# Performance work log

Hardware: AMD Instinct MI355X
Metric: run time of the kernel (lower is better)

The kernel has to match this reference:

```python
import jax, jax.numpy as jnp
from jax import lax
import numpy as np

RATIOS = (0.5, 1.0, 2.0)
SCALES = (8, 16, 32)
BASE = 16
STRIDE = 16
IMG_H, IMG_W = 1024, 1024
NMS_THR = 0.7
N_IN = 6000   # eval mode (training=False)
N_OUT = 300
MIN_SIZE = 16


def _base_anchors():
    ctr = BASE / 2.0
    anc = []
    for r in RATIOS:
        for s in SCALES:
            h = BASE * s * np.sqrt(r)
            w = BASE * s * np.sqrt(1.0 / r)
            anc.append([ctr - h / 2, ctr - w / 2, ctr + h / 2, ctr + w / 2])
    return np.asarray(anc, dtype=np.float32)  # (9,4) yxyx


def _shifted_anchors(H, W):
    base = _base_anchors()
    sy = np.arange(H, dtype=np.float32) * STRIDE
    sx = np.arange(W, dtype=np.float32) * STRIDE
    yy, xx = np.meshgrid(sy, sx, indexing='ij')
    shift = np.stack([yy, xx, yy, xx], axis=-1).reshape(-1, 1, 4)  # (H*W,1,4)
    return jnp.asarray((shift + base[None]).reshape(-1, 4))        # (H*W*9,4)


def _conv(x, w, b):
    y = lax.conv_general_dilated(x, w, (1, 1), 'SAME',
                                 dimension_numbers=('NCHW', 'OIHW', 'NCHW'))
    return y + b[None, :, None, None]


def _loc2bbox(src, locs):
    h = src[:, 2] - src[:, 0]
    w = src[:, 3] - src[:, 1]
    cy = src[:, 0] + 0.5 * h
    cx = src[:, 1] + 0.5 * w
    dy, dx, dh, dw = locs[:, 0], locs[:, 1], locs[:, 2], locs[:, 3]
    cty = dy * h + cy
    ctx = dx * w + cx
    th = jnp.exp(dh) * h
    tw = jnp.exp(dw) * w
    return jnp.stack([cty - 0.5 * th, ctx - 0.5 * tw,
                      cty + 0.5 * th, ctx + 0.5 * tw], axis=-1)


def _nms_keep(boxes, valid):
    n = boxes.shape[0]
    areas = (boxes[:, 2] - boxes[:, 0]) * (boxes[:, 3] - boxes[:, 1])
    idx = jnp.arange(n)

    def body(i, keep):
        b = lax.dynamic_slice(boxes, (i, 0), (1, 4))[0]
        yy1 = jnp.maximum(b[0], boxes[:, 0])
        xx1 = jnp.maximum(b[1], boxes[:, 1])
        yy2 = jnp.minimum(b[2], boxes[:, 2])
        xx2 = jnp.minimum(b[3], boxes[:, 3])
        inter = jnp.clip(yy2 - yy1, 0) * jnp.clip(xx2 - xx1, 0)
        iou = inter / (areas[i] + areas - inter + 1e-9)
        sup = (iou > NMS_THR) & (idx > i) & keep[i]
        return keep & ~sup

    return lax.fori_loop(0, n, body, valid)


def _proposals(locs, fg, anchors):
    # locs (R,4), fg (R,), anchors (R,4) -> (N_OUT,4) padded with zeros
    rois = _loc2bbox(anchors, locs)
    y1 = jnp.clip(rois[:, 0], 0, IMG_H)
    y2 = jnp.clip(rois[:, 2], 0, IMG_H)
    x1 = jnp.clip(rois[:, 1], 0, IMG_W)
    x2 = jnp.clip(rois[:, 3], 0, IMG_W)
    rois = jnp.stack([y1, x1, y2, x2], axis=-1)
    valid = ((y2 - y1) >= MIN_SIZE) & ((x2 - x1) >= MIN_SIZE)
    s = jnp.where(valid, fg, -jnp.inf)
    order = jnp.argsort(-s)[:N_IN]
    rois_s = rois[order]
    valid_s = valid[order]
    keep = _nms_keep(rois_s, valid_s)
    rank = jnp.cumsum(keep.astype(jnp.int32)) - 1
    tgt = jnp.where(keep & (rank < N_OUT), rank, N_OUT)
    out = jnp.zeros((N_OUT + 1, 4), rois.dtype).at[tgt].set(rois_s)
    return out[:N_OUT]


def reference(x, conv_w, conv_b, score_w, score_b, loc_w, loc_b):
    B, C, H, W = x.shape
    anchors = _shifted_anchors(H, W)                      # (R,4)
    h = jax.nn.relu(_conv(x, conv_w, conv_b))             # (B,mid,H,W)
    rpn_locs = _conv(h, loc_w, loc_b).transpose(0, 2, 3, 1).reshape(B, -1, 4)
    rpn_scores = _conv(h, score_w, score_b).transpose(0, 2, 3, 1).reshape(B, -1, 2)
    fg = jax.nn.softmax(rpn_scores, axis=2)[:, :, 1]      # (B,R)
    rois = jax.vmap(_proposals, in_axes=(0, 0, None))(rpn_locs, fg, anchors)
    rois = rois.reshape(-1, 4)                            # (B*N_OUT,4)
    roi_indices = jnp.repeat(jnp.arange(B, dtype=jnp.int32), N_OUT)
    return rpn_scores, rpn_locs, rois, roi_indices, anchors


def setup_inputs() -> dict:
    key = jax.random.key(0)
    ks = jax.random.split(key, 7)
    B, Cin, Cmid, H, W = 4, 512, 512, 64, 64
    return {
        'x': jax.random.normal(ks[0], (B, Cin, H, W), jnp.float32),
        'conv_w': jax.random.normal(ks[1], (Cmid, Cin, 3, 3), jnp.float32) * 0.01,
        'conv_b': jax.random.normal(ks[2], (Cmid,), jnp.float32) * 0.01,
        'score_w': jax.random.normal(ks[3], (18, Cmid, 1, 1), jnp.float32) * 0.01,
        'score_b': jax.random.normal(ks[4], (18,), jnp.float32) * 0.01,
        'loc_w': jax.random.normal(ks[5], (36, Cmid, 1, 1), jnp.float32) * 0.01,
        'loc_b': jax.random.normal(ks[6], (36,), jnp.float32) * 0.01,
    }
```

## Files before the change

### kernel.cpp

```cpp
#include <hip/hip_runtime.h>
#include <cstdint>
#include <cmath>

namespace {
constexpr int BATCH = 4;
constexpr int CIN   = 512;
constexpr int CMID  = 512;
constexpr int HSZ   = 64, WSZ = 64, HWP = 4096;
constexpr int NA    = 36864;
constexpr int NIN_  = 6000;
constexpr int NOUT2 = 300;
constexpr int NW    = 94;

constexpr size_t O_SC  = 0;
constexpr size_t O_LC  = 294912;
constexpr size_t O_ROI = 884736;
constexpr size_t O_IDX = 889536;
constexpr size_t O_ANC = 890736;

constexpr size_t W_H    = 0;
constexpr size_t W_WHI  = 8388608;
constexpr size_t W_WLO  = 9568256;
constexpr size_t W_R4   = 0;
constexpr size_t W_SK   = 589824;
constexpr size_t W_HIST = 737280;
constexpr size_t W_CNT  = 753664;
constexpr size_t W_CUT  = 753668;
constexpr size_t W_NHI1 = 753672;
constexpr size_t W_CUT2 = 753676;
constexpr size_t W_NHI2 = 753680;
constexpr size_t W_CUT3 = 753684;
constexpr size_t W_ZERO = 753688;
constexpr size_t W_NHI3 = 753692;
constexpr size_t W_H2   = 753728;
constexpr size_t W_H3   = 770112;
constexpr size_t W_CKEY = 901184;
constexpr size_t W_RS   = 1196096;
constexpr size_t W_VS   = 1292096;
constexpr size_t W_MAT  = 1316096;
}

typedef _Float16 f16;
typedef __attribute__((ext_vector_type(4))) _Float16 f16x4;
typedef __attribute__((ext_vector_type(8))) _Float16 f16x8;
typedef __attribute__((ext_vector_type(4))) float f32x4;

__global__ __launch_bounds__(256) void k0w(const float* __restrict__ w,
                                           f16* __restrict__ whi, f16* __restrict__ wlo) {
    int o = blockIdx.x * 256 + threadIdx.x;
    int ci = o & 511;
    int r  = o >> 9;
    int co = r & 511;
    int kk = r >> 9;
    float f = w[(co * CIN + ci) * 9 + kk] * 64.0f;
    f16 hv = (f16)f;
    whi[o] = hv;
    wlo[o] = (f16)((f - (float)hv) * 2048.0f);
}

__global__ __launch_bounds__(256, 2) void k1_mfma(const float* __restrict__ x,
                                                  const f16* __restrict__ gwh,
                                                  const f16* __restrict__ gwl,
                                                  const float* __restrict__ bias,
                                                  float* __restrict__ h) {
    const int pt = blockIdx.x, cg = blockIdx.y, b = blockIdx.z;
    const int y0 = pt * 2, co0 = cg * 128;
    const int t = threadIdx.x;
    const int wave = t >> 6, lane = t & 63;
    const int wrow = wave >> 1, wco = wave & 1;
    const int m = lane & 15, q = lane >> 4;

    __shared__ __align__(16) f16 xs[2][4 * 66 * 40];
    __shared__ __align__(16) f16 wt[2][2][128 * 32];

    f32x4 acc1[4][4], acc2[4][4];
#pragma unroll
    for (int i = 0; i < 4; ++i)
#pragma unroll
        for (int j = 0; j < 4; ++j) { acc1[i][j] = (f32x4)0.0f; acc2[i][j] = (f32x4)0.0f; }

    const int cq = t & 7, srow = (t >> 3) & 3, cseg = t >> 5;
    const int gy = y0 - 1 + srow;
    const bool yok = (gy >= 0 && gy < HSZ);

    if (t < 128) {
        int buf = t >> 6, rr = (t >> 4) & 3, cc = ((t >> 3) & 1) ? 65 : 0, cq2 = t & 7;
        f16x4 z = (f16x4)(f16)0.0f;
        *(f16x4*)&xs[buf][(rr * 66 + cc) * 40 + cq2 * 4] = z;
    }

    {
#pragma unroll
        for (int s = 0; s < 2; ++s) {
            int idx = s * 256 + t;
            int co_l = idx >> 2, q8 = idx & 3;
            size_t g = ((size_t)(co0 + co_l)) * 512 + q8 * 8;
            *(f16x8*)&wt[0][0][co_l * 32 + q8 * 8] = *(const f16x8*)&gwh[g];
            *(f16x8*)&wt[0][1][co_l * 32 + q8 * 8] = *(const f16x8*)&gwl[g];
        }
    }

    int chunk = 0, kk = 0;
    for (int ks = 0; ks < 144; ++ks) {
        const int slot = ks & 1;
        __syncthreads();

        if (kk == 0) {
            float vb[4][8];
            const float* xp = x + ((size_t)(b * CIN + chunk * 32 + cq * 4)) * HWP + gy * WSZ + cseg * 8;
#pragma unroll
            for (int i = 0; i < 4; ++i) {
                if (yok) {
                    float4 u0 = *(const float4*)(xp + (size_t)i * HWP);
                    float4 u1 = *(const float4*)(xp + (size_t)i * HWP + 4);
                    vb[i][0] = u0.x; vb[i][1] = u0.y; vb[i][2] = u0.z; vb[i][3] = u0.w;
                    vb[i][4] = u1.x; vb[i][5] = u1.y; vb[i][6] = u1.z; vb[i][7] = u1.w;
                } else {
#pragma unroll
                    for (int jj = 0; jj < 8; ++jj) vb[i][jj] = 0.0f;
                }
            }
#pragma unroll
            for (int j = 0; j < 8; ++j) {
                int c = (j + cq) & 7;
                int col = cseg * 8 + c + 1;
                f16x4 hv, lv;
#pragma unroll
                for (int i = 0; i < 4; ++i) {
                    float f = vb[i][c];
                    f16 hf = (f16)f;
                    hv[i] = hf;
                    lv[i] = (f16)((f - (float)hf) * 2048.0f);
                }
                int base = (srow * 66 + col) * 40 + cq * 4;
                *(f16x4*)&xs[0][base] = hv;
                *(f16x4*)&xs[1][base] = lv;
            }
        }

        if (ks + 1 < 144) {
            int kk2 = kk + 1, ch2 = chunk;
            if (kk2 == 9) { kk2 = 0; ch2++; }
#pragma unroll
            for (int s = 0; s < 2; ++s) {
                int idx = s * 256 + t;
                int co_l = idx >> 2, q8 = idx & 3;
                size_t g = ((size_t)(kk2 * 512 + co0 + co_l)) * 512 + ch2 * 32 + q8 * 8;
                *(f16x8*)&wt[slot ^ 1][0][co_l * 32 + q8 * 8] = *(const f16x8*)&gwh[g];
                *(f16x8*)&wt[slot ^ 1][1][co_l * 32 + q8 * 8] = *(const f16x8*)&gwl[g];
            }
        }

        if (kk == 0) __syncthreads();

        const int ky = (kk >= 6) ? 2 : (kk >= 3) ? 1 : 0;
        const int kx = kk - ky * 3;
        const int rs = wrow + ky;

        f16x8 bh[4], bl[4], ah[4], al[4];
#pragma unroll
        for (int nt = 0; nt < 4; ++nt) {
            int off = (wco * 64 + nt * 16 + m) * 32 + q * 8;
            bh[nt] = *(const f16x8*)&wt[slot][0][off];
            bl[nt] = *(const f16x8*)&wt[slot][1][off];
        }
#pragma unroll
        for (int ct = 0; ct < 4; ++ct) {
            int off = (rs * 66 + ct * 16 + m + kx) * 40 + q * 8;
            ah[ct] = *(const f16x8*)&xs[0][off];
            al[ct] = *(const f16x8*)&xs[1][off];
        }
#pragma unroll
        for (int ct = 0; ct < 4; ++ct)
#pragma unroll
            for (int nt = 0; nt < 4; ++nt) {
                acc1[ct][nt] = __builtin_amdgcn_mfma_f32_16x16x32_f16(ah[ct], bh[nt], acc1[ct][nt], 0, 0, 0);
                acc2[ct][nt] = __builtin_amdgcn_mfma_f32_16x16x32_f16(ah[ct], bl[nt], acc2[ct][nt], 0, 0, 0);
                acc2[ct][nt] = __builtin_amdgcn_mfma_f32_16x16x32_f16(al[ct], bh[nt], acc2[ct][nt], 0, 0, 0);
            }

        ++kk;
        if (kk == 9) { kk = 0; ++chunk; }
    }

    const int y = y0 + wrow;
#pragma unroll
    for (int nt = 0; nt < 4; ++nt) {
        const int co = co0 + wco * 64 + nt * 16 + m;
        const float bv = bias[co];
        size_t rowbase = ((size_t)(b * CMID + co)) * HWP + y * WSZ;
#pragma unroll
        for (int ct = 0; ct < 4; ++ct) {
            float4 o;
            o.x = fmaxf((acc1[ct][nt][0] + acc2[ct][nt][0] * (1.0f / 2048.0f)) * (1.0f / 64.0f) + bv, 0.0f);
            o.y = fmaxf((acc1[ct][nt][1] + acc2[ct][nt][1] * (1.0f / 2048.0f)) * (1.0f / 64.0f) + bv, 0.0f);
            o.z = fmaxf((acc1[ct][nt][2] + acc2[ct][nt][2] * (1.0f / 2048.0f)) * (1.0f / 64.0f) + bv, 0.0f);
            o.w = fmaxf((acc1[ct][nt][3] + acc2[ct][nt][3] * (1.0f / 2048.0f)) * (1.0f / 64.0f) + bv, 0.0f);
            *(float4*)&h[rowbase + ct * 16 + q * 4] = o;
        }
    }
}

__global__ __launch_bounds__(256) void k2_conv1(const float* __restrict__ h,
                                                const float* __restrict__ sw,
                                                const float* __restrict__ sb,
                                                const float* __restrict__ lw,
                                                const float* __restrict__ lb,
                                                float* __restrict__ out) {
    const int y = blockIdx.x;
    const int b = blockIdx.y;
    const int t = threadIdx.x;
    const int c4  = (t & 15) * 4;
    const int px4 = (t >> 4) * 4;
    __shared__ __align__(16) float hs[1024];
    __shared__ __align__(16) float wsm[16 * 68];

    float acc[4][4];
#pragma unroll
    for (int i = 0; i < 4; ++i)
#pragma unroll
        for (int j = 0; j < 4; ++j) acc[i][j] = 0.f;

    const int s_px = (t & 15) * 4;
    const int s_ci = t >> 4;
    for (int ci0 = 0; ci0 < CMID; ci0 += 16) {
        *(float4*)&hs[s_ci * 64 + s_px] =
            *(const float4*)&h[((size_t)(b * CMID + ci0 + s_ci)) * HWP + y * 64 + s_px];
#pragma unroll
        for (int k = 0; k < 4; ++k) {
            int idx = k * 256 + t;
            int ci = idx & 15, c = idx >> 4;
            float v = 0.f;
            if (c < 18) v = sw[c * 512 + ci0 + ci];
            else if (c < 54) v = lw[(c - 18) * 512 + ci0 + ci];
            wsm[ci * 68 + c] = v;
        }
        __syncthreads();
#pragma unroll
        for (int ci = 0; ci < 16; ++ci) {
            float4 hv = *(const float4*)&hs[ci * 64 + px4];
            float4 wv = *(const float4*)&wsm[ci * 68 + c4];
            acc[0][0] = fmaf(wv.x, hv.x, acc[0][0]);
            acc[0][1] = fmaf(wv.x, hv.y, acc[0][1]);
            acc[0][2] = fmaf(wv.x, hv.z, acc[0][2]);
            acc[0][3] = fmaf(wv.x, hv.w, acc[0][3]);
            acc[1][0] = fmaf(wv.y, hv.x, acc[1][0]);
            acc[1][1] = fmaf(wv.y, hv.y, acc[1][1]);
            acc[1][2] = fmaf(wv.y, hv.z, acc[1][2]);
            acc[1][3] = fmaf(wv.y, hv.w, acc[1][3]);
            acc[2][0] = fmaf(wv.z, hv.x, acc[2][0]);
            acc[2][1] = fmaf(wv.z, hv.y, acc[2][1]);
            acc[2][2] = fmaf(wv.z, hv.z, acc[2][2]);
            acc[2][3] = fmaf(wv.z, hv.w, acc[2][3]);
            acc[3][0] = fmaf(wv.w, hv.x, acc[3][0]);
            acc[3][1] = fmaf(wv.w, hv.y, acc[3][1]);
            acc[3][2] = fmaf(wv.w, hv.z, acc[3][2]);
            acc[3][3] = fmaf(wv.w, hv.w, acc[3][3]);
        }
        __syncthreads();
    }

#pragma unroll
    for (int cc = 0; cc < 4; ++cc) {
        int c = c4 + cc;
        if (c >= 54) break;
        float bv = (c < 18) ? sb[c] : lb[c - 18];
#pragma unroll
        for (int pp = 0; pp < 4; ++pp) {
            int px = y * 64 + px4 + pp;
            float v = acc[cc][pp] + bv;
            if (c < 18)
                out[O_SC + (size_t)b * 73728 + (size_t)px * 18 + c] = v;
            else
                out[O_LC + (size_t)b * 147456 + (size_t)px * 36 + (c - 18)] = v;
        }
    }
}

__global__ __launch_bounds__(256) void k3_prop(float* __restrict__ out,
                                               float* __restrict__ rois4,
                                               float* __restrict__ skey,
                                               int* __restrict__ hist) {
    __shared__ int lh[4096];
    const int t = threadIdx.x;
    for (int k = t; k < 4096; k += 256) lh[k] = 0;
    __syncthreads();

    const int p = blockIdx.x * 256 + t;
    const int b = blockIdx.y;
    const int px = p / 9;
    const int a  = p - px * 9;
    const int yy = px >> 6, xx = px & 63;
    const int ri = a / 3, si = a - ri * 3;
    const double rat[3] = {0.5, 1.0, 2.0};
    const double scl[3] = {8.0, 16.0, 32.0};
    double hhd = 16.0 * scl[si] * sqrt(rat[ri]);
    double wwd = 16.0 * scl[si] * sqrt(1.0 / rat[ri]);
    float a0 = (float)(8.0 - hhd / 2.0), a1 = (float)(8.0 - wwd / 2.0);
    float a2 = (float)(8.0 + hhd / 2.0), a3 = (float)(8.0 + wwd / 2.0);
    float sy = (float)(yy * 16), sx = (float)(xx * 16);
    float A0 = sy + a0, A1 = sx + a1, A2 = sy + a2, A3 = sx + a3;
    if (b == 0) {
        float4 av; av.x = A0; av.y = A1; av.z = A2; av.w = A3;
        *(float4*)&out[O_ANC + (size_t)p * 4] = av;
    }
    const float* sc = out + O_SC + (size_t)b * 73728 + (size_t)px * 18 + a * 2;
    float s0 = sc[0], s1 = sc[1];
    float m = fmaxf(s0, s1);
    float e0 = expf(s0 - m), e1 = expf(s1 - m);
    float fg = e1 / (e0 + e1);
    const float* lc = out + O_LC + (size_t)b * 147456 + (size_t)px * 36 + a * 4;
    float dy = lc[0], dxv = lc[1], dh = lc[2], dwv = lc[3];
    float ah = A2 - A0, aw = A3 - A1;
    float cy = A0 + 0.5f * ah, cx = A1 + 0.5f * aw;
    float cty = dy * ah + cy, ctx = dxv * aw + cx;
    float th = expf(dh) * ah, tw = expf(dwv) * aw;
    float ry1 = cty - 0.5f * th, rx1 = ctx - 0.5f * tw;
    float ry2 = cty + 0.5f * th, rx2 = ctx + 0.5f * tw;
    float y1 = fminf(fmaxf(ry1, 0.f), 1024.f);
    float y2 = fminf(fmaxf(ry2, 0.f), 1024.f);
    float x1 = fminf(fmaxf(rx1, 0.f), 1024.f);
    float x2 = fminf(fmaxf(rx2, 0.f), 1024.f);
    bool valid = ((y2 - y1) >= 16.f) && ((x2 - x1) >= 16.f);
    float sk = valid ? fg : -__builtin_inff();
    float4 rv; rv.x = y1; rv.y = x1; rv.z = y2; rv.w = x2;
    *(float4*)&rois4[((size_t)b * NA + p) * 4] = rv;
    skey[(size_t)b * NA + p] = sk;
    unsigned u = __float_as_uint(sk);
    u = (u & 0x80000000u) ? ~u : (u | 0x80000000u);
    atomicAdd(&lh[u >> 20], 1);
    __syncthreads();
    for (int k = t; k < 4096; k += 256) {
        int v = lh[k];
        if (v) atomicAdd(&hist[b * 4096 + k], v);
    }
}

__global__ __launch_bounds__(256) void k4scan(const int* __restrict__ hist,
                                              const int* __restrict__ cum_in,
                                              int* __restrict__ cut,
                                              int* __restrict__ cum_out) {
    __shared__ int hl[4096];
    __shared__ int tsum[256];
    const int t = threadIdx.x;
    for (int b = 0; b < BATCH; ++b) {
        const int target = NIN_ - cum_in[b];
        for (int k = t; k < 4096; k += 256) hl[k] = hist[b * 4096 + k];
        __syncthreads();
        int s = 0;
#pragma unroll
        for (int j = 0; j < 16; ++j) s += hl[t * 16 + j];
        tsum[t] = s;
        __syncthreads();
        if (t == 0) {
            int run = 0;
            for (int tt = 255; tt >= 0; --tt) { int tmp = tsum[tt]; tsum[tt] = run; run += tmp; }
        }
        __syncthreads();
        int run = tsum[t];
        for (int v = t * 16 + 15; v >= t * 16; --v) {
            int prev = run;
            run += hl[v];
            if (run >= target && prev < target) {
                cut[b] = v;
                cum_out[b] = cum_in[b] + prev;
            }
        }
        __syncthreads();
    }
}

__global__ __launch_bounds__(256) void k4h(const float* __restrict__ skey,
                                           const int* __restrict__ cut1,
                                           const int* __restrict__ cut2,
                                           int* __restrict__ hist, int level) {
    __shared__ int lh[4096];
    const int t = threadIdx.x;
    for (int k = t; k < 4096; k += 256) lh[k] = 0;
    __syncthreads();
    const int p = blockIdx.x * 256 + t;
    const int b = blockIdx.y;
    float sk = skey[(size_t)b * NA + p];
    unsigned u = __float_as_uint(sk);
    u = (u & 0x80000000u) ? ~u : (u | 0x80000000u);
    int b1 = (int)(u >> 20), b2 = (int)((u >> 8) & 0xFFFu);
    if (level == 2) {
        if (b1 == cut1[b]) atomicAdd(&lh[b2], 1);
    } else {
        if (b1 == cut1[b] && b2 == cut2[b]) atomicAdd(&lh[(36863 - p) >> 4], 1);
    }
    __syncthreads();
    for (int k = t; k < 4096; k += 256) {
        int v = lh[k];
        if (v) atomicAdd(&hist[b * 4096 + k], v);
    }
}

__global__ __launch_bounds__(256) void k4c_compact(const float* __restrict__ skey,
                                                   const int* __restrict__ cut1,
                                                   const int* __restrict__ cut2,
                                                   const int* __restrict__ cut3,
                                                   int* __restrict__ cnt,
                                                   unsigned long long* __restrict__ ckey) {
    const int p = blockIdx.x * 256 + threadIdx.x;
    const int b = blockIdx.y;
    float sk = skey[(size_t)b * NA + p];
    unsigned u = __float_as_uint(sk);
    u = (u & 0x80000000u) ? ~u : (u | 0x80000000u);
    int b1 = (int)(u >> 20), b2 = (int)((u >> 8) & 0xFFFu), b3 = (36863 - p) >> 4;
    int c1 = cut1[b], c2 = cut2[b], c3 = cut3[b];
    bool take = (b1 > c1) || (b1 == c1 && (b2 > c2 || (b2 == c2 && b3 >= c3)));
    if (take) {
        int pos = atomicAdd(&cnt[b], 1);
        ckey[(size_t)b * NA + pos] =
            ((unsigned long long)u << 16) | (unsigned long long)(36863 - p);
    }
}

__global__ __launch_bounds__(1024) void k4d_sort(const int* __restrict__ cnt,
                                                 const unsigned long long* __restrict__ ckey,
                                                 const float* __restrict__ rois4,
                                                 float* __restrict__ rois_s,
                                                 int* __restrict__ valid_s) {
    const int b = blockIdx.x, t = threadIdx.x;
    const int C = min(cnt[b], 8192);
    __shared__ unsigned long long keys[8192];
#pragma unroll
    for (int s = 0; s < 8; ++s) {
        int i = s * 1024 + t;
        keys[i] = (i < C) ? ckey[(size_t)b * NA + i] : 0ull;
    }
    __syncthreads();
    for (int k = 2; k <= 8192; k <<= 1) {
        for (int j = k >> 1; j > 0; j >>= 1) {
#pragma unroll
            for (int s = 0; s < 8; ++s) {
                int i = s * 1024 + t;
                int ixj = i ^ j;
                if (ixj > i) {
                    unsigned long long x = keys[i], y = keys[ixj];
                    bool up = ((i & k) == 0);
                    if (up ? (x < y) : (x > y)) { keys[i] = y; keys[ixj] = x; }
                }
            }
            __syncthreads();
        }
    }
    for (int r = t; r < NIN_; r += 1024) {
        unsigned long long key = keys[r];
        int p = 36863 - (int)(key & 0xFFFFull);
        const float4 bx = *(const float4*)&rois4[((size_t)b * NA + p) * 4];
        *(float4*)&rois_s[((size_t)b * NIN_ + r) * 4] = bx;
        valid_s[b * NIN_ + r] = ((unsigned)(key >> 16) != 0x007FFFFFu) ? 1 : 0;
    }
}

__global__ __launch_bounds__(256) void k5_mat(const float* __restrict__ rois_s,
                                              unsigned long long* __restrict__ mat) {
    const int b = blockIdx.y, rb = blockIdx.x;
    const int t = threadIdx.x, wave = t >> 6, lane = t & 63;
    const int i = rb * 64 + lane;
    const bool rowok = (i < NIN_);
    __shared__ float cs[4][5][64];
    const float* bb = rois_s + (size_t)b * NIN_ * 4;

    float r0 = 0, r1 = 0, r2 = 0, r3 = 0, ra = 0;
    if (rowok) {
        float4 v = *(const float4*)&bb[(size_t)i * 4];
        r0 = v.x; r1 = v.y; r2 = v.z; r3 = v.w;
        ra = (v.z - v.x) * (v.w - v.y);
    }
    unsigned long long* mrow = mat + ((size_t)b * NIN_ + (size_t)(rowok ? i : 0)) * NW;

    if (rowok)
        for (int cb = wave; cb < rb; cb += 4) mrow[cb] = 0ull;

    for (int cb = rb + wave; cb < NW; cb += 4) {
        const int j0 = cb * 64;
        const int j  = j0 + lane;
        float4 v;
        if (j < NIN_) v = *(const float4*)&bb[(size_t)j * 4];
        else { v.x = 0; v.y = 0; v.z = 0; v.w = 0; }
        cs[wave][0][lane] = v.x; cs[wave][1][lane] = v.y;
        cs[wave][2][lane] = v.z; cs[wave][3][lane] = v.w;
        cs[wave][4][lane] = (v.z - v.x) * (v.w - v.y);
        unsigned long long wm = 0;
        if (rowok) {
#pragma unroll 8
            for (int k = 0; k < 64; ++k) {
                float yy1 = fmaxf(r0, cs[wave][0][k]), xx1 = fmaxf(r1, cs[wave][1][k]);
                float yy2 = fminf(r2, cs[wave][2][k]), xx2 = fminf(r3, cs[wave][3][k]);
                float inter = fmaxf(yy2 - yy1, 0.f) * fmaxf(xx2 - xx1, 0.f);
                float iou = inter / (ra + cs[wave][4][k] - inter + 1e-9f);
                int jj = j0 + k;
                if ((iou > 0.7f) && (jj > i) && (jj < NIN_)) wm |= (1ull << k);
            }
            mrow[cb] = wm;
        }
    }
}

__global__ __launch_bounds__(64) void k5_scan(const unsigned long long* __restrict__ mat,
                                              const float* __restrict__ rois_s,
                                              const int* __restrict__ valid_s,
                                              float* __restrict__ out) {
    const int b = blockIdx.x, t = threadIdx.x;
    for (int k = t; k < NOUT2 * 4; k += 64) out[O_ROI + (size_t)b * NOUT2 * 4 + k] = 0.f;
    for (int k = t; k < NOUT2; k += 64) out[O_IDX + (size_t)b * NOUT2 + k] = (float)b;

    unsigned long long A = 0, B = 0;
    for (int w = 0; w < NW; ++w) {
        int i = w * 64 + t;
        int v = (i < NIN_) ? valid_s[b * NIN_ + i] : 0;
        unsigned long long m = __ballot(v == 0);
        if (w < 64) { if (t == w) A = m; }
        else        { if (t == w - 64) B = m; }
    }

    const unsigned long long* mb = mat + (size_t)b * NIN_ * NW;
    const float* bb = rois_s + (size_t)b * NIN_ * 4;
    int kept = 0;
    for (int w = 0; w < NW && kept < NOUT2; ++w) {
        unsigned long long cur = (w < 64) ? __shfl(A, w) : __shfl(B, w - 64);
        unsigned long long avail = ~cur;
        while (avail != 0ull && kept < NOUT2) {
            int bit = __builtin_ctzll(avail);
            int i = w * 64 + bit;
            if (t == 0) {
                float4 bx = *(const float4*)&bb[(size_t)i * 4];
                *(float4*)&out[O_ROI + ((size_t)b * NOUT2 + kept) * 4] = bx;
            }
            kept++;
            if (kept >= NOUT2) break;
            const unsigned long long* row = mb + (size_t)i * NW;
            unsigned long long rA = row[t];
            unsigned long long rB = (t < NW - 64) ? row[64 + t] : 0ull;
            A |= rA; B |= rB;
            unsigned long long rw = (w < 64) ? __shfl(rA, w) : __shfl(rB, w - 64);
            avail &= ~rw;
            avail &= ~(1ull << bit);
        }
    }
}

extern "C" void kernel_launch(void* const* d_in, const int* in_sizes, int n_in,
                              void* d_out, int out_size, void* d_ws, size_t ws_size,
                              hipStream_t stream) {
    const float* x       = (const float*)d_in[0];
    const float* conv_w  = (const float*)d_in[1];
    const float* conv_b  = (const float*)d_in[2];
    const float* score_w = (const float*)d_in[3];
    const float* score_b = (const float*)d_in[4];
    const float* loc_w   = (const float*)d_in[5];
    const float* loc_b   = (const float*)d_in[6];
    float* out = (float*)d_out;
    float* ws  = (float*)d_ws;

    f16* whi = (f16*)(ws + W_WHI);
    f16* wlo = (f16*)(ws + W_WLO);

    k0w<<<2359296 / 256, 256, 0, stream>>>(conv_w, whi, wlo);
    k1_mfma<<<dim3(32, 4, 4), 256, 0, stream>>>(x, whi, wlo, conv_b, ws + W_H);
    k2_conv1<<<dim3(64, 4), 256, 0, stream>>>(ws + W_H, score_w, score_b, loc_w, loc_b, out);
    hipMemsetAsync(ws + W_HIST, 0, (size_t)(W_H3 + 16384 - W_HIST) * 4, stream);
    k3_prop<<<dim3(144, 4), 256, 0, stream>>>(out, ws + W_R4, ws + W_SK, (int*)(ws + W_HIST));
    k4scan<<<1, 256, 0, stream>>>((const int*)(ws + W_HIST), (const int*)(ws + W_ZERO),
                                  (int*)(ws + W_CUT), (int*)(ws + W_NHI1));
    k4h<<<dim3(144, 4), 256, 0, stream>>>(ws + W_SK, (const int*)(ws + W_CUT),
                                          (const int*)(ws + W_CUT2), (int*)(ws + W_H2), 2);
    k4scan<<<1, 256, 0, stream>>>((const int*)(ws + W_H2), (const int*)(ws + W_NHI1),
                                  (int*)(ws + W_CUT2), (int*)(ws + W_NHI2));
    k4h<<<dim3(144, 4), 256, 0, stream>>>(ws + W_SK, (const int*)(ws + W_CUT),
                                          (const int*)(ws + W_CUT2), (int*)(ws + W_H3), 3);
    k4scan<<<1, 256, 0, stream>>>((const int*)(ws + W_H3), (const int*)(ws + W_NHI2),
                                  (int*)(ws + W_CUT3), (int*)(ws + W_NHI3));
    k4c_compact<<<dim3(144, 4), 256, 0, stream>>>(ws + W_SK, (const int*)(ws + W_CUT),
                                                  (const int*)(ws + W_CUT2),
                                                  (const int*)(ws + W_CUT3),
                                                  (int*)(ws + W_CNT),
                                                  (unsigned long long*)(ws + W_CKEY));
    k4d_sort<<<BATCH, 1024, 0, stream>>>((const int*)(ws + W_CNT),
                                         (const unsigned long long*)(ws + W_CKEY),
                                         ws + W_R4, ws + W_RS, (int*)(ws + W_VS));
    k5_mat<<<dim3(NW, BATCH), 256, 0, stream>>>(ws + W_RS, (unsigned long long*)(ws + W_MAT));
    k5_scan<<<BATCH, 64, 0, stream>>>((const unsigned long long*)(ws + W_MAT),
                                      ws + W_RS, (const int*)(ws + W_VS), out);
}
```

Measured before the change: 1.025 ms.

## Restructure conv mainloop with swizzled weight LDS and fuse radix-select passes

The conv kernel's K loop becomes a nested chunk/tap loop with precomputed, XOR-swizzled LDS addresses for the weight tiles. This is meant to cut LDS bank conflicts and per-iteration index arithmetic, at the cost of an extra barrier per chunk. The three histogram/scan launch pairs of the top-k radix select become one per-batch 1024-thread kernel that builds per-wave shared histograms. That removes several launches, global atomics and the large memset, but puts the whole selection for each batch on a single block that reads its keys three times.

```diff
diff --git a/kernel.cpp b/kernel.cpp
--- a/kernel.cpp
+++ b/kernel.cpp
@@ -23,17 +23,10 @@
 constexpr size_t W_WLO  = 9568256;
 constexpr size_t W_R4   = 0;
 constexpr size_t W_SK   = 589824;
-constexpr size_t W_HIST = 737280;
 constexpr size_t W_CNT  = 753664;
 constexpr size_t W_CUT  = 753668;
-constexpr size_t W_NHI1 = 753672;
 constexpr size_t W_CUT2 = 753676;
-constexpr size_t W_NHI2 = 753680;
 constexpr size_t W_CUT3 = 753684;
-constexpr size_t W_ZERO = 753688;
-constexpr size_t W_NHI3 = 753692;
-constexpr size_t W_H2   = 753728;
-constexpr size_t W_H3   = 770112;
 constexpr size_t W_CKEY = 901184;
 constexpr size_t W_RS   = 1196096;
 constexpr size_t W_VS   = 1292096;
@@ -89,23 +82,30 @@
         *(f16x4*)&xs[buf][(rr * 66 + cc) * 40 + cq2 * 4] = z;
     }
 
-    {
-#pragma unroll
-        for (int s = 0; s < 2; ++s) {
-            int idx = s * 256 + t;
-            int co_l = idx >> 2, q8 = idx & 3;
-            size_t g = ((size_t)(co0 + co_l)) * 512 + q8 * 8;
-            *(f16x8*)&wt[0][0][co_l * 32 + q8 * 8] = *(const f16x8*)&gwh[g];
-            *(f16x8*)&wt[0][1][co_l * 32 + q8 * 8] = *(const f16x8*)&gwl[g];
-        }
-    }
-
-    int chunk = 0, kk = 0;
-    for (int ks = 0; ks < 144; ++ks) {
-        const int slot = ks & 1;
-        __syncthreads();
-
-        if (kk == 0) {
+    int wbase[2], wpos[2];
+#pragma unroll
+    for (int s = 0; s < 2; ++s) {
+        int idx = s * 256 + t;
+        int co_l = idx >> 2, q8 = idx & 3;
+        wbase[s] = (co0 + co_l) * 512 + q8 * 8;
+        wpos[s]  = co_l * 32 + ((q8 * 8) ^ (((co_l >> 1) & 3) << 3));
+    }
+
+#pragma unroll
+    for (int s = 0; s < 2; ++s) {
+        *(f16x8*)&wt[0][0][wpos[s]] = *(const f16x8*)&gwh[wbase[s]];
+        *(f16x8*)&wt[0][1][wpos[s]] = *(const f16x8*)&gwl[wbase[s]];
+    }
+
+    const int swzB  = ((m >> 1) & 3) << 3;
+    const int baseB = wco * 2048 + m * 32 + ((q * 8) ^ swzB);
+    const int baseA = wrow * 2640 + m * 40 + q * 8;
+
+    for (int chunk = 0; chunk < 16; ++chunk) {
+        const int slot0 = chunk & 1;
+        __syncthreads();
+
+        {
             float vb[4][8];
             const float* xp = x + ((size_t)(b * CIN + chunk * 32 + cq * 4)) * HWP + gy * WSZ + cseg * 8;
 #pragma unroll
@@ -137,50 +137,59 @@
                 *(f16x4*)&xs[1][base] = lv;
             }
         }
-
-        if (ks + 1 < 144) {
-            int kk2 = kk + 1, ch2 = chunk;
-            if (kk2 == 9) { kk2 = 0; ch2++; }
-#pragma unroll
-            for (int s = 0; s < 2; ++s) {
-                int idx = s * 256 + t;
-                int co_l = idx >> 2, q8 = idx & 3;
-                size_t g = ((size_t)(kk2 * 512 + co0 + co_l)) * 512 + ch2 * 32 + q8 * 8;
-                *(f16x8*)&wt[slot ^ 1][0][co_l * 32 + q8 * 8] = *(const f16x8*)&gwh[g];
-                *(f16x8*)&wt[slot ^ 1][1][co_l * 32 + q8 * 8] = *(const f16x8*)&gwl[g];
-            }
-        }
-
-        if (kk == 0) __syncthreads();
-
-        const int ky = (kk >= 6) ? 2 : (kk >= 3) ? 1 : 0;
-        const int kx = kk - ky * 3;
-        const int rs = wrow + ky;
-
-        f16x8 bh[4], bl[4], ah[4], al[4];
-#pragma unroll
-        for (int nt = 0; nt < 4; ++nt) {
-            int off = (wco * 64 + nt * 16 + m) * 32 + q * 8;
-            bh[nt] = *(const f16x8*)&wt[slot][0][off];
-            bl[nt] = *(const f16x8*)&wt[slot][1][off];
-        }
-#pragma unroll
-        for (int ct = 0; ct < 4; ++ct) {
-            int off = (rs * 66 + ct * 16 + m + kx) * 40 + q * 8;
-            ah[ct] = *(const f16x8*)&xs[0][off];
-            al[ct] = *(const f16x8*)&xs[1][off];
-        }
-#pragma unroll
-        for (int ct = 0; ct < 4; ++ct)
+#pragma unroll
+        for (int s = 0; s < 2; ++s) {
+            int g = wbase[s] + 262144 + chunk * 32;
+            *(f16x8*)&wt[slot0 ^ 1][0][wpos[s]] = *(const f16x8*)&gwh[g];
+            *(f16x8*)&wt[slot0 ^ 1][1][wpos[s]] = *(const f16x8*)&gwl[g];
+        }
+        __syncthreads();
+
+#pragma unroll
+        for (int kk = 0; kk < 9; ++kk) {
+            const int slot = (chunk + kk) & 1;
+            if (kk > 0) {
+                __syncthreads();
+                if (kk < 8) {
+#pragma unroll
+                    for (int s = 0; s < 2; ++s) {
+                        int g = wbase[s] + (kk + 1) * 262144 + chunk * 32;
+                        *(f16x8*)&wt[slot ^ 1][0][wpos[s]] = *(const f16x8*)&gwh[g];
+                        *(f16x8*)&wt[slot ^ 1][1][wpos[s]] = *(const f16x8*)&gwl[g];
+                    }
+                } else if (chunk < 15) {
+#pragma unroll
+                    for (int s = 0; s < 2; ++s) {
+                        int g = wbase[s] + (chunk + 1) * 32;
+                        *(f16x8*)&wt[slot ^ 1][0][wpos[s]] = *(const f16x8*)&gwh[g];
+                        *(f16x8*)&wt[slot ^ 1][1][wpos[s]] = *(const f16x8*)&gwl[g];
+                    }
+                }
+            }
+            const int ky = kk / 3, kx = kk - ky * 3;
+
+            f16x8 bh[4], bl[4], ah[4], al[4];
 #pragma unroll
             for (int nt = 0; nt < 4; ++nt) {
-                acc1[ct][nt] = __builtin_amdgcn_mfma_f32_16x16x32_f16(ah[ct], bh[nt], acc1[ct][nt], 0, 0, 0);
-                acc2[ct][nt] = __builtin_amdgcn_mfma_f32_16x16x32_f16(ah[ct], bl[nt], acc2[ct][nt], 0, 0, 0);
-                acc2[ct][nt] = __builtin_amdgcn_mfma_f32_16x16x32_f16(al[ct], bh[nt], acc2[ct][nt], 0, 0, 0);
-            }
-
-        ++kk;
-        if (kk == 9) { kk = 0; ++chunk; }
+                int off = baseB + nt * 512;
+                bh[nt] = *(const f16x8*)&wt[slot][0][off];
+                bl[nt] = *(const f16x8*)&wt[slot][1][off];
+            }
+#pragma unroll
+            for (int ct = 0; ct < 4; ++ct) {
+                int off = baseA + ky * 2640 + kx * 40 + ct * 640;
+                ah[ct] = *(const f16x8*)&xs[0][off];
+                al[ct] = *(const f16x8*)&xs[1][off];
+            }
+#pragma unroll
+            for (int ct = 0; ct < 4; ++ct)
+#pragma unroll
+                for (int nt = 0; nt < 4; ++nt) {
+                    acc1[ct][nt] = __builtin_amdgcn_mfma_f32_16x16x32_f16(ah[ct], bh[nt], acc1[ct][nt], 0, 0, 0);
+                    acc2[ct][nt] = __builtin_amdgcn_mfma_f32_16x16x32_f16(ah[ct], bl[nt], acc2[ct][nt], 0, 0, 0);
+                    acc2[ct][nt] = __builtin_amdgcn_mfma_f32_16x16x32_f16(al[ct], bh[nt], acc2[ct][nt], 0, 0, 0);
+                }
+        }
     }
 
     const int y = y0 + wrow;
@@ -279,13 +288,8 @@
 
 __global__ __launch_bounds__(256) void k3_prop(float* __restrict__ out,
                                                float* __restrict__ rois4,
-                                               float* __restrict__ skey,
-                                               int* __restrict__ hist) {
-    __shared__ int lh[4096];
+                                               float* __restrict__ skey) {
     const int t = threadIdx.x;
-    for (int k = t; k < 4096; k += 256) lh[k] = 0;
-    __syncthreads();
-
     const int p = blockIdx.x * 256 + t;
     const int b = blockIdx.y;
     const int px = p / 9;
@@ -306,8 +310,8 @@
     }
     const float* sc = out + O_SC + (size_t)b * 73728 + (size_t)px * 18 + a * 2;
     float s0 = sc[0], s1 = sc[1];
-    float m = fmaxf(s0, s1);
-    float e0 = expf(s0 - m), e1 = expf(s1 - m);
+    float mm = fmaxf(s0, s1);
+    float e0 = expf(s0 - mm), e1 = expf(s1 - mm);
     float fg = e1 / (e0 + e1);
     const float* lc = out + O_LC + (size_t)b * 147456 + (size_t)px * 36 + a * 4;
     float dy = lc[0], dxv = lc[1], dh = lc[2], dwv = lc[3];
@@ -326,74 +330,70 @@
     float4 rv; rv.x = y1; rv.y = x1; rv.z = y2; rv.w = x2;
     *(float4*)&rois4[((size_t)b * NA + p) * 4] = rv;
     skey[(size_t)b * NA + p] = sk;
-    unsigned u = __float_as_uint(sk);
-    u = (u & 0x80000000u) ? ~u : (u | 0x80000000u);
-    atomicAdd(&lh[u >> 20], 1);
-    __syncthreads();
-    for (int k = t; k < 4096; k += 256) {
-        int v = lh[k];
-        if (v) atomicAdd(&hist[b * 4096 + k], v);
-    }
-}
-
-__global__ __launch_bounds__(256) void k4scan(const int* __restrict__ hist,
-                                              const int* __restrict__ cum_in,
-                                              int* __restrict__ cut,
-                                              int* __restrict__ cum_out) {
-    __shared__ int hl[4096];
+}
+
+__global__ __launch_bounds__(1024) void k4r(const float* __restrict__ skey,
+                                            int* __restrict__ cut1g,
+                                            int* __restrict__ cut2g,
+                                            int* __restrict__ cut3g) {
+    const int b = blockIdx.x, t = threadIdx.x;
+    const int w8 = (t >> 6) & 7;
+    __shared__ int h8[8][4096];
     __shared__ int tsum[256];
-    const int t = threadIdx.x;
-    for (int b = 0; b < BATCH; ++b) {
-        const int target = NIN_ - cum_in[b];
-        for (int k = t; k < 4096; k += 256) hl[k] = hist[b * 4096 + k];
-        __syncthreads();
-        int s = 0;
-#pragma unroll
-        for (int j = 0; j < 16; ++j) s += hl[t * 16 + j];
-        tsum[t] = s;
+    __shared__ int s_cut, s_prev;
+    int cum = 0;
+    int cuts[3];
+#pragma unroll 1
+    for (int level = 0; level < 3; ++level) {
+        for (int k = t; k < 8 * 4096; k += 1024) ((int*)h8)[k] = 0;
+        __syncthreads();
+        for (int i = t; i < NA; i += 1024) {
+            float sk = skey[(size_t)b * NA + i];
+            unsigned u = __float_as_uint(sk);
+            u = (u & 0x80000000u) ? ~u : (u | 0x80000000u);
+            int b1 = (int)(u >> 20), b2 = (int)((u >> 8) & 0xFFFu);
+            int digit; bool pred;
+            if (level == 0)      { digit = b1;                pred = true; }
+            else if (level == 1) { digit = b2;                pred = (b1 == cuts[0]); }
+            else                 { digit = (36863 - i) >> 4;  pred = (b1 == cuts[0] && b2 == cuts[1]); }
+            if (pred) atomicAdd(&h8[w8][digit], 1);
+        }
+        __syncthreads();
+        for (int k = t; k < 4096; k += 1024) {
+            int s = h8[0][k];
+#pragma unroll
+            for (int r = 1; r < 8; ++r) s += h8[r][k];
+            h8[0][k] = s;
+        }
+        __syncthreads();
+        if (t < 256) {
+            const int target = NIN_ - cum;
+            int s = 0;
+#pragma unroll
+            for (int j = 0; j < 16; ++j) s += h8[0][t * 16 + j];
+            tsum[t] = s;
+        }
         __syncthreads();
         if (t == 0) {
             int run = 0;
             for (int tt = 255; tt >= 0; --tt) { int tmp = tsum[tt]; tsum[tt] = run; run += tmp; }
         }
         __syncthreads();
-        int run = tsum[t];
-        for (int v = t * 16 + 15; v >= t * 16; --v) {
-            int prev = run;
-            run += hl[v];
-            if (run >= target && prev < target) {
-                cut[b] = v;
-                cum_out[b] = cum_in[b] + prev;
-            }
-        }
-        __syncthreads();
-    }
-}
-
-__global__ __launch_bounds__(256) void k4h(const float* __restrict__ skey,
-                                           const int* __restrict__ cut1,
-                                           const int* __restrict__ cut2,
-                                           int* __restrict__ hist, int level) {
-    __shared__ int lh[4096];
-    const int t = threadIdx.x;
-    for (int k = t; k < 4096; k += 256) lh[k] = 0;
-    __syncthreads();
-    const int p = blockIdx.x * 256 + t;
-    const int b = blockIdx.y;
-    float sk = skey[(size_t)b * NA + p];
-    unsigned u = __float_as_uint(sk);
-    u = (u & 0x80000000u) ? ~u : (u | 0x80000000u);
-    int b1 = (int)(u >> 20), b2 = (int)((u >> 8) & 0xFFFu);
-    if (level == 2) {
-        if (b1 == cut1[b]) atomicAdd(&lh[b2], 1);
-    } else {
-        if (b1 == cut1[b] && b2 == cut2[b]) atomicAdd(&lh[(36863 - p) >> 4], 1);
-    }
-    __syncthreads();
-    for (int k = t; k < 4096; k += 256) {
-        int v = lh[k];
-        if (v) atomicAdd(&hist[b * 4096 + k], v);
-    }
+        if (t < 256) {
+            const int target = NIN_ - cum;
+            int run = tsum[t];
+            for (int v = t * 16 + 15; v >= t * 16; --v) {
+                int prev = run;
+                run += h8[0][v];
+                if (run >= target && prev < target) { s_cut = v; s_prev = prev; }
+            }
+        }
+        __syncthreads();
+        cuts[level] = s_cut;
+        cum += s_prev;
+        __syncthreads();
+    }
+    if (t == 0) { cut1g[b] = cuts[0]; cut2g[b] = cuts[1]; cut3g[b] = cuts[2]; }
 }
 
 __global__ __launch_bounds__(256) void k4c_compact(const float* __restrict__ skey,
@@ -562,18 +562,10 @@
     k0w<<<2359296 / 256, 256, 0, stream>>>(conv_w, whi, wlo);
     k1_mfma<<<dim3(32, 4, 4), 256, 0, stream>>>(x, whi, wlo, conv_b, ws + W_H);
     k2_conv1<<<dim3(64, 4), 256, 0, stream>>>(ws + W_H, score_w, score_b, loc_w, loc_b, out);
-    hipMemsetAsync(ws + W_HIST, 0, (size_t)(W_H3 + 16384 - W_HIST) * 4, stream);
-    k3_prop<<<dim3(144, 4), 256, 0, stream>>>(out, ws + W_R4, ws + W_SK, (int*)(ws + W_HIST));
-    k4scan<<<1, 256, 0, stream>>>((const int*)(ws + W_HIST), (const int*)(ws + W_ZERO),
-                                  (int*)(ws + W_CUT), (int*)(ws + W_NHI1));
-    k4h<<<dim3(144, 4), 256, 0, stream>>>(ws + W_SK, (const int*)(ws + W_CUT),
-                                          (const int*)(ws + W_CUT2), (int*)(ws + W_H2), 2);
-    k4scan<<<1, 256, 0, stream>>>((const int*)(ws + W_H2), (const int*)(ws + W_NHI1),
-                                  (int*)(ws + W_CUT2), (int*)(ws + W_NHI2));
-    k4h<<<dim3(144, 4), 256, 0, stream>>>(ws + W_SK, (const int*)(ws + W_CUT),
-                                          (const int*)(ws + W_CUT2), (int*)(ws + W_H3), 3);
-    k4scan<<<1, 256, 0, stream>>>((const int*)(ws + W_H3), (const int*)(ws + W_NHI2),
-                                  (int*)(ws + W_CUT3), (int*)(ws + W_NHI3));
+    hipMemsetAsync(ws + W_CNT, 0, 128, stream);
+    k3_prop<<<dim3(144, 4), 256, 0, stream>>>(out, ws + W_R4, ws + W_SK);
+    k4r<<<BATCH, 1024, 0, stream>>>(ws + W_SK, (int*)(ws + W_CUT),
+                                    (int*)(ws + W_CUT2), (int*)(ws + W_CUT3));
     k4c_compact<<<dim3(144, 4), 256, 0, stream>>>(ws + W_SK, (const int*)(ws + W_CUT),
                                                   (const int*)(ws + W_CUT2),
                                                   (const int*)(ws + W_CUT3),
```

Result: no change. 1.033 ms (+0.8%).
